# Performance work log

Measured on AMD Instinct MI355X. Metric: run time of the kernel, lower is better.

The kernel has to match this reference:

```python
import jax, jax.numpy as jnp
import numpy as np

N_CLUSTERS = 100
ALPHA = 1.0
NDF = 256
IN_DIM = 1024 * 8 * 8  # i3d_nch * os * os
BN, SN = 32, 64


def setup_inputs() -> dict:
    key = jax.random.key(0)
    k1, k2, k3, k4 = jax.random.split(key, 4)
    z_roi = jax.random.normal(k1, (BN, SN, IN_DIM), dtype=jnp.float32)
    mask = jnp.ones((BN, SN), dtype=bool)
    w_emb = jax.random.normal(k2, (IN_DIM, NDF), dtype=jnp.float32) * 0.02
    b_emb = jnp.zeros((NDF,), dtype=jnp.float32)
    centroids = jax.random.normal(k3, (N_CLUSTERS, NDF), dtype=jnp.float32)
    return {"z_roi": z_roi, "mask": mask, "w_emb": w_emb,
            "b_emb": b_emb, "centroids": centroids}


def _student_t(z, centroids):
    # z: [bn, sn, d]; centroids: [K, d]
    # pairwise L2 distance (NOT squared, matching torch.linalg.vector_norm)
    d2 = ((z * z).sum(-1, keepdims=True)
          + (centroids * centroids).sum(-1)
          - 2.0 * jnp.einsum("bsd,kd->bsk", z, centroids))  # [bn, sn, K]
    dist = jnp.sqrt(jnp.clip(d2, 0.0))
    s_tmp = (1.0 + dist / ALPHA) ** (-(ALPHA + 1.0) / 2.0)
    return s_tmp / s_tmp.sum(-1, keepdims=True)


def reference(z_roi, mask, w_emb, b_emb, centroids):
    # visual embedding: Linear(i3d_nch*os*os -> ndf)
    z = jnp.einsum("bsi,io->bso", z_roi, w_emb) + b_emb  # [bn, sn, ndf]
    m = mask[..., None]
    s = jnp.where(m, _student_t(z, centroids), 0.0)       # [bn, sn, K]
    z_all = jnp.where(m, z, 0.0)                           # detached copy in torch
    c = jnp.argmax(s, axis=2)                              # [bn, sn]
    return z_all, s, c
```

## Files before the change

kernel.cpp:

```cpp
#include <hip/hip_runtime.h>
#include <math.h>

#define MROWS 2048
#define NCOLS 256
#define KDIM  65536
#define NCLU  100

#define BM 128
#define BN 128
#define BK 32
#define SPLITK 16
#define KCHUNK (KDIM / SPLITK)
#define SA 132
#define SB 128

#define BMT 128
#define BNT 128
#define BKT 32
#define LDT 40

typedef _Float16 half8  __attribute__((ext_vector_type(8)));
typedef _Float16 half4v __attribute__((ext_vector_type(4)));
typedef float    f32x4  __attribute__((ext_vector_type(4)));

__global__ __launch_bounds__(256, 4)
void prep_b_kernel(const float* __restrict__ B,
                   _Float16* __restrict__ Bth, _Float16* __restrict__ Btl)
{
    __shared__ float T[64][65];
    const int t  = threadIdx.x;
    const int k0 = blockIdx.x * 64;
    const int n0 = blockIdx.y * 64;

    {
        const int kl = t >> 4;
        const int n4 = (t & 15) * 4;
        #pragma unroll
        for (int i = 0; i < 4; ++i) {
            const float4 v = *(const float4*)(B + (size_t)(k0 + kl + 16 * i) * NCOLS + n0 + n4);
            T[kl + 16 * i][n4 + 0] = v.x;
            T[kl + 16 * i][n4 + 1] = v.y;
            T[kl + 16 * i][n4 + 2] = v.z;
            T[kl + 16 * i][n4 + 3] = v.w;
        }
    }
    __syncthreads();
    {
        const int nl = t >> 2;
        const int kc = (t & 3) * 16;
        half8 h0, h1, l0, l1;
        #pragma unroll
        for (int j = 0; j < 8; ++j) {
            float v = T[kc + j][nl];
            _Float16 h = (_Float16)v;
            h0[j] = h; l0[j] = (_Float16)(v - (float)h);
            v = T[kc + 8 + j][nl];
            h = (_Float16)v;
            h1[j] = h; l1[j] = (_Float16)(v - (float)h);
        }
        const size_t off = (size_t)(n0 + nl) * KDIM + k0 + kc;
        *(half8*)(Bth + off)     = h0;
        *(half8*)(Bth + off + 8) = h1;
        *(half8*)(Btl + off)     = l0;
        *(half8*)(Btl + off + 8) = l1;
    }
}

__global__ __launch_bounds__(256, 1)
void gemm_mfma_kernel(const float* __restrict__ A,
                      const _Float16* __restrict__ Bth,
                      const _Float16* __restrict__ Btl,
                      float* __restrict__ C)
{
    __shared__ _Float16 As [BMT][LDT];
    __shared__ _Float16 Bhs[BNT][LDT];
    __shared__ _Float16 Bls[BNT][LDT];

    const int t    = threadIdx.x;
    const int lane = t & 63;
    const int wid  = t >> 6;
    const int wm   = wid >> 1;
    const int wn   = wid & 1;

    const int bm = blockIdx.x;
    const int bn = blockIdx.y;
    const int ks = blockIdx.z;

    const float*    Ab  = A   + (size_t)bm * BMT * KDIM + (size_t)ks * KCHUNK;
    const _Float16* Bhb = Bth + (size_t)bn * BNT * KDIM + (size_t)ks * KCHUNK;
    const _Float16* Blb = Btl + (size_t)bn * BNT * KDIM + (size_t)ks * KCHUNK;

    const int am  = t >> 3;
    const int ak  = (t & 7) * 4;
    const int bnr = t >> 2;
    const int bk  = (t & 3) * 8;

    f32x4 acc[4][4] = {};

    for (int kk = 0; kk < KCHUNK; kk += BKT) {
        __syncthreads();
        #pragma unroll
        for (int i = 0; i < 4; ++i) {
            const float4 v = *(const float4*)(Ab + (size_t)(am + 32 * i) * KDIM + kk + ak);
            half4v h;
            h[0] = (_Float16)v.x; h[1] = (_Float16)v.y;
            h[2] = (_Float16)v.z; h[3] = (_Float16)v.w;
            *(half4v*)&As[am + 32 * i][ak] = h;
        }
        #pragma unroll
        for (int i = 0; i < 2; ++i) {
            const int n = bnr + 64 * i;
            *(half8*)&Bhs[n][bk] = *(const half8*)(Bhb + (size_t)n * KDIM + kk + bk);
            *(half8*)&Bls[n][bk] = *(const half8*)(Blb + (size_t)n * KDIM + kk + bk);
        }
        __syncthreads();

        const int r16 = lane & 15;
        const int k8  = (lane >> 4) * 8;
        half8 av[4], bh[4], bl[4];
        #pragma unroll
        for (int mf = 0; mf < 4; ++mf)
            av[mf] = *(const half8*)&As[wm * 64 + mf * 16 + r16][k8];
        #pragma unroll
        for (int nf = 0; nf < 4; ++nf) {
            bh[nf] = *(const half8*)&Bhs[wn * 64 + nf * 16 + r16][k8];
            bl[nf] = *(const half8*)&Bls[wn * 64 + nf * 16 + r16][k8];
        }
        #pragma unroll
        for (int mf = 0; mf < 4; ++mf)
            #pragma unroll
            for (int nf = 0; nf < 4; ++nf) {
                acc[mf][nf] = __builtin_amdgcn_mfma_f32_16x16x32_f16(av[mf], bh[nf], acc[mf][nf], 0, 0, 0);
                acc[mf][nf] = __builtin_amdgcn_mfma_f32_16x16x32_f16(av[mf], bl[nf], acc[mf][nf], 0, 0, 0);
            }
    }

    const int row0 = bm * BMT + wm * 64 + (lane >> 4) * 4;
    const int col0 = bn * BNT + wn * 64 + (lane & 15);
    #pragma unroll
    for (int mf = 0; mf < 4; ++mf)
        #pragma unroll
        for (int nf = 0; nf < 4; ++nf)
            #pragma unroll
            for (int r = 0; r < 4; ++r)
                atomicAdd(&C[(size_t)(row0 + mf * 16 + r) * NCOLS + col0 + nf * 16],
                          acc[mf][nf][r]);
}

__global__ __launch_bounds__(256, 2)
void gemm_splitk_kernel(const float* __restrict__ A, const float* __restrict__ B,
                        float* __restrict__ C)
{
    __shared__ float As[BK][SA];
    __shared__ float Bs[BK][SB];

    const int t  = threadIdx.x;
    const int tx = t & 15;
    const int ty = t >> 4;

    const int bm = blockIdx.x;
    const int bn = blockIdx.y;
    const int bs = blockIdx.z;

    const float* Ab = A + (size_t)bm * BM * KDIM + (size_t)bs * KCHUNK;
    const float* Bb = B + (size_t)bs * KCHUNK * NCOLS + bn * BN;

    const int arow = t >> 3;
    const int akf4 = t & 7;
    const int bkr  = t >> 5;
    const int bnf4 = t & 31;

    float acc[8][8];
    #pragma unroll
    for (int i = 0; i < 8; ++i)
        #pragma unroll
        for (int j = 0; j < 8; ++j) acc[i][j] = 0.f;

    for (int kk = 0; kk < KCHUNK; kk += BK) {
        #pragma unroll
        for (int i = 0; i < 4; ++i) {
            const int r = arow + 32 * i;
            const float4 v = *(const float4*)(Ab + (size_t)r * KDIM + kk + akf4 * 4);
            As[akf4 * 4 + 0][r] = v.x;
            As[akf4 * 4 + 1][r] = v.y;
            As[akf4 * 4 + 2][r] = v.z;
            As[akf4 * 4 + 3][r] = v.w;
        }
        #pragma unroll
        for (int i = 0; i < 4; ++i) {
            const int r = bkr + 8 * i;
            *(float4*)&Bs[r][bnf4 * 4] =
                *(const float4*)(Bb + (size_t)(kk + r) * NCOLS + bnf4 * 4);
        }
        __syncthreads();

        #pragma unroll 8
        for (int k = 0; k < BK; ++k) {
            float a[8], b[8];
            *(float4*)&a[0] = *(const float4*)&As[k][ty * 4];
            *(float4*)&a[4] = *(const float4*)&As[k][64 + ty * 4];
            *(float4*)&b[0] = *(const float4*)&Bs[k][tx * 4];
            *(float4*)&b[4] = *(const float4*)&Bs[k][64 + tx * 4];
            #pragma unroll
            for (int i = 0; i < 8; ++i)
                #pragma unroll
                for (int j = 0; j < 8; ++j)
                    acc[i][j] = fmaf(a[i], b[j], acc[i][j]);
        }
        __syncthreads();
    }

    #pragma unroll
    for (int i = 0; i < 8; ++i) {
        const int row = bm * BM + ty * 4 + (i & 3) + 64 * (i >> 2);
        #pragma unroll
        for (int j = 0; j < 8; ++j) {
            const int col = bn * BN + tx * 4 + (j & 3) + 64 * (j >> 2);
            atomicAdd(&C[(size_t)row * NCOLS + col], acc[i][j]);
        }
    }
}

#define RPB 8

__global__ __launch_bounds__(256, 1)
void student_t_kernel(float* __restrict__ zbuf,
                      const int* __restrict__ mask,
                      const float* __restrict__ b_emb,
                      const float* __restrict__ cent,
                      float* __restrict__ s_out,
                      float* __restrict__ c_out)
{
    __shared__ float cs[50][257];
    __shared__ float zs[RPB][256];
    __shared__ float stbuf[RPB][128];
    __shared__ float c2[NCLU];
    __shared__ float z2s[RPB];
    __shared__ float redbuf[4];
    __shared__ float r_sum, r_idx;

    const int t    = threadIdx.x;
    const int wid  = t >> 6;
    const int lane = t & 63;
    const int row0 = blockIdx.x * RPB;

    const float bt = b_emb[t];

    if (t >= 100 && t < 128) {
        #pragma unroll
        for (int r = 0; r < RPB; ++r) stbuf[r][t] = 0.f;
    }

    for (int r = 0; r < RPB; ++r) {
        const int row = row0 + r;
        const float z = zbuf[(size_t)row * NCOLS + t] + bt;
        const bool m = mask[row] != 0;
        zbuf[(size_t)row * NCOLS + t] = m ? z : 0.f;
        zs[r][t] = z;
        float v = z * z;
        #pragma unroll
        for (int off = 32; off > 0; off >>= 1) v += __shfl_down(v, off, 64);
        if (lane == 0) redbuf[wid] = v;
        __syncthreads();
        if (t == 0) z2s[r] = redbuf[0] + redbuf[1] + redbuf[2] + redbuf[3];
        __syncthreads();
    }

    for (int ch = 0; ch < 2; ++ch) {
        const int kbase = ch * 50;
        for (int i = t; i < 50 * 256; i += 256) {
            const int k = i >> 8;
            const int d = i & 255;
            cs[k][d] = cent[(size_t)(kbase + k) * 256 + d];
        }
        __syncthreads();
        if (t < 50) {
            float s = 0.f;
            for (int d = 0; d < 256; ++d) s = fmaf(cs[t][d], cs[t][d], s);
            c2[kbase + t] = s;
        }
        __syncthreads();
        for (int rp = 0; rp < RPB / 2; ++rp) {
            if (t < 100) {
                const int r = rp * 2 + t / 50;
                const int k = t % 50;
                float dot = 0.f;
                for (int d = 0; d < 256; ++d)
                    dot = fmaf(zs[r][d], cs[k][d], dot);
                const float d2   = z2s[r] + c2[kbase + k] - 2.f * dot;
                const float dist = sqrtf(fmaxf(d2, 0.f));
                stbuf[r][kbase + k] = 1.f / (1.f + dist);
            }
        }
        __syncthreads();
    }

    for (int r = 0; r < RPB; ++r) {
        const int row = row0 + r;
        if (wid == 0) {
            const float v1 = stbuf[r][lane];
            const float v2 = stbuf[r][lane + 64];
            float sv = v1 + v2;
            #pragma unroll
            for (int off = 32; off > 0; off >>= 1) sv += __shfl_down(sv, off, 64);
            float mv; int mi;
            if (v2 > v1) { mv = v2; mi = lane + 64; } else { mv = v1; mi = lane; }
            #pragma unroll
            for (int off = 32; off > 0; off >>= 1) {
                const float ov = __shfl_down(mv, off, 64);
                const int   oi = __shfl_down(mi, off, 64);
                if (ov > mv || (ov == mv && oi < mi)) { mv = ov; mi = oi; }
            }
            if (lane == 0) { r_sum = sv; r_idx = (float)mi; }
        }
        __syncthreads();
        const bool m = mask[row] != 0;
        if (t < NCLU) s_out[(size_t)row * NCLU + t] = m ? stbuf[r][t] / r_sum : 0.f;
        if (t == 0)   c_out[row] = m ? r_idx : 0.f;
        __syncthreads();
    }
}

extern "C" void kernel_launch(void* const* d_in, const int* in_sizes, int n_in,
                              void* d_out, int out_size, void* d_ws, size_t ws_size,
                              hipStream_t stream)
{
    const float* z_roi = (const float*)d_in[0];
    const int*   mask  = (const int*)d_in[1];
    const float* w_emb = (const float*)d_in[2];
    const float* b_emb = (const float*)d_in[3];
    const float* cent  = (const float*)d_in[4];

    float* out   = (float*)d_out;
    float* z_all = out;
    float* s_out = out + (size_t)MROWS * NCOLS;
    float* c_out = s_out + (size_t)MROWS * NCLU;

    hipMemsetAsync(z_all, 0, (size_t)MROWS * NCOLS * sizeof(float), stream);

    const size_t bt_elems = (size_t)NCOLS * KDIM;
    const size_t ws_need  = bt_elems * 2 * sizeof(_Float16);

    if (ws_size >= ws_need) {
        _Float16* bth = (_Float16*)d_ws;
        _Float16* btl = bth + bt_elems;
        prep_b_kernel<<<dim3(KDIM / 64, NCOLS / 64), 256, 0, stream>>>(w_emb, bth, btl);
        gemm_mfma_kernel<<<dim3(MROWS / BMT, NCOLS / BNT, SPLITK), 256, 0, stream>>>(
            z_roi, bth, btl, z_all);
    } else {
        gemm_splitk_kernel<<<dim3(MROWS / BM, NCOLS / BN, SPLITK), 256, 0, stream>>>(
            z_roi, w_emb, z_all);
    }

    student_t_kernel<<<dim3(MROWS / RPB), 256, 0, stream>>>(z_all, mask, b_emb, cent,
                                                            s_out, c_out);
}
```

Before: 908.0 us.

## Double-buffer MFMA GEMM with pre-tiled swizzled B and direct global-to-LDS loads

The prep kernel now writes W as pre-tiled, XOR-swizzled 16KB tiles holding interleaved fp16 hi and lo parts. The GEMM loads each tile straight into LDS with global_load_lds and double-buffers both A and B. This lets the next K-step's loads overlap the current MFMAs and needs one barrier per step instead of two. Occupancy is raised to 2 blocks per CU, at the cost of more LDS per block.

```diff
diff --git a/kernel.cpp b/kernel.cpp
--- a/kernel.cpp
+++ b/kernel.cpp
@@ -17,64 +17,67 @@
 #define BMT 128
 #define BNT 128
 #define BKT 32
+#define NSTEP (KCHUNK / BKT)
 #define LDT 40
+#define BTILE 16384
 
 typedef _Float16 half8  __attribute__((ext_vector_type(8)));
 typedef _Float16 half4v __attribute__((ext_vector_type(4)));
 typedef float    f32x4  __attribute__((ext_vector_type(4)));
 
+#define GLD_LDS16(g, l) __builtin_amdgcn_global_load_lds(                      \
+    (__attribute__((address_space(1))) void*)(g),                              \
+    (__attribute__((address_space(3))) void*)(l), 16, 0, 0)
+
 __global__ __launch_bounds__(256, 4)
-void prep_b_kernel(const float* __restrict__ B,
-                   _Float16* __restrict__ Bth, _Float16* __restrict__ Btl)
-{
-    __shared__ float T[64][65];
-    const int t  = threadIdx.x;
-    const int k0 = blockIdx.x * 64;
-    const int n0 = blockIdx.y * 64;
-
-    {
-        const int kl = t >> 4;
-        const int n4 = (t & 15) * 4;
-        #pragma unroll
-        for (int i = 0; i < 4; ++i) {
-            const float4 v = *(const float4*)(B + (size_t)(k0 + kl + 16 * i) * NCOLS + n0 + n4);
-            T[kl + 16 * i][n4 + 0] = v.x;
-            T[kl + 16 * i][n4 + 1] = v.y;
-            T[kl + 16 * i][n4 + 2] = v.z;
-            T[kl + 16 * i][n4 + 3] = v.w;
-        }
+void prep_b_kernel(const float* __restrict__ B, unsigned char* __restrict__ Bws)
+{
+    __shared__ float Ts[BKT][132];
+    const int t    = threadIdx.x;
+    const int step = blockIdx.x;
+    const int ks   = blockIdx.y;
+    const int bnb  = blockIdx.z;
+
+    const int kbase = ks * KCHUNK + step * BKT;
+    const int nbase = bnb * 128;
+
+    #pragma unroll
+    for (int r = 0; r < 4; ++r) {
+        const int fidx = r * 256 + t;
+        const int k  = fidx >> 5;
+        const int c4 = fidx & 31;
+        const float4 v = *(const float4*)(B + (size_t)(kbase + k) * NCOLS + nbase + c4 * 4);
+        *(float4*)&Ts[k][c4 * 4] = v;
     }
     __syncthreads();
-    {
-        const int nl = t >> 2;
-        const int kc = (t & 3) * 16;
-        half8 h0, h1, l0, l1;
+
+    unsigned char* outT = Bws + (size_t)((bnb * SPLITK + ks) * NSTEP + step) * BTILE;
+    #pragma unroll
+    for (int r = 0; r < 4; ++r) {
+        const int oidx = r * 256 + t;
+        const int n  = oidx >> 3;
+        const int X  = oidx & 7;
+        const int LX = X ^ (n & 7);
+        const int mtx = LX >> 2;
+        const int kb  = (LX & 3) * 8;
+        half8 hv;
         #pragma unroll
         for (int j = 0; j < 8; ++j) {
-            float v = T[kc + j][nl];
-            _Float16 h = (_Float16)v;
-            h0[j] = h; l0[j] = (_Float16)(v - (float)h);
-            v = T[kc + 8 + j][nl];
-            h = (_Float16)v;
-            h1[j] = h; l1[j] = (_Float16)(v - (float)h);
-        }
-        const size_t off = (size_t)(n0 + nl) * KDIM + k0 + kc;
-        *(half8*)(Bth + off)     = h0;
-        *(half8*)(Bth + off + 8) = h1;
-        *(half8*)(Btl + off)     = l0;
-        *(half8*)(Btl + off + 8) = l1;
-    }
-}
-
-__global__ __launch_bounds__(256, 1)
+            const float v = Ts[kb + j][n];
+            const _Float16 h = (_Float16)v;
+            hv[j] = mtx ? (_Float16)(v - (float)h) : h;
+        }
+        *(half8*)(outT + n * 128 + X * 16) = hv;
+    }
+}
+
+__global__ __launch_bounds__(256, 2)
 void gemm_mfma_kernel(const float* __restrict__ A,
-                      const _Float16* __restrict__ Bth,
-                      const _Float16* __restrict__ Btl,
+                      const unsigned char* __restrict__ Bws,
                       float* __restrict__ C)
 {
-    __shared__ _Float16 As [BMT][LDT];
-    __shared__ _Float16 Bhs[BNT][LDT];
-    __shared__ _Float16 Bls[BNT][LDT];
+    __shared__ _Float16 As[2][BMT][LDT];
+    __shared__ __align__(16) unsigned char Bs[2][BTILE];
 
     const int t    = threadIdx.x;
     const int lane = t & 63;
@@ -82,49 +85,72 @@
     const int wm   = wid >> 1;
     const int wn   = wid & 1;
 
-    const int bm = blockIdx.x;
-    const int bn = blockIdx.y;
-    const int ks = blockIdx.z;
-
-    const float*    Ab  = A   + (size_t)bm * BMT * KDIM + (size_t)ks * KCHUNK;
-    const _Float16* Bhb = Bth + (size_t)bn * BNT * KDIM + (size_t)ks * KCHUNK;
-    const _Float16* Blb = Btl + (size_t)bn * BNT * KDIM + (size_t)ks * KCHUNK;
+    const int bm  = blockIdx.x;
+    const int bnb = blockIdx.y;
+    const int ks  = blockIdx.z;
+
+    const float* Ab = A + (size_t)bm * BMT * KDIM + (size_t)ks * KCHUNK;
+    const unsigned char* Bb = Bws + (size_t)((bnb * SPLITK + ks) * NSTEP) * BTILE;
 
     const int am  = t >> 3;
-    const int ak  = (t & 7) * 4;
-    const int bnr = t >> 2;
-    const int bk  = (t & 3) * 8;
+    const int akf = (t & 7) * 4;
+
+    const int r16  = lane & 15;
+    const int kb16 = lane >> 4;
+
+    int bhoff[4], bloff[4];
+    #pragma unroll
+    for (int nf = 0; nf < 4; ++nf) {
+        const int n    = wn * 64 + nf * 16 + r16;
+        const int mask = (n & 7) << 4;
+        bhoff[nf] = n * 128 + ((kb16 * 16) ^ mask);
+        bloff[nf] = n * 128 + ((64 + kb16 * 16) ^ mask);
+    }
 
     f32x4 acc[4][4] = {};
-
-    for (int kk = 0; kk < KCHUNK; kk += BKT) {
-        __syncthreads();
-        #pragma unroll
-        for (int i = 0; i < 4; ++i) {
-            const float4 v = *(const float4*)(Ab + (size_t)(am + 32 * i) * KDIM + kk + ak);
-            half4v h;
-            h[0] = (_Float16)v.x; h[1] = (_Float16)v.y;
-            h[2] = (_Float16)v.z; h[3] = (_Float16)v.w;
-            *(half4v*)&As[am + 32 * i][ak] = h;
-        }
-        #pragma unroll
-        for (int i = 0; i < 2; ++i) {
-            const int n = bnr + 64 * i;
-            *(half8*)&Bhs[n][bk] = *(const half8*)(Bhb + (size_t)n * KDIM + kk + bk);
-            *(half8*)&Bls[n][bk] = *(const half8*)(Blb + (size_t)n * KDIM + kk + bk);
-        }
-        __syncthreads();
-
-        const int r16 = lane & 15;
-        const int k8  = (lane >> 4) * 8;
+    float4 pA[4];
+
+    #pragma unroll
+    for (int i = 0; i < 4; ++i)
+        pA[i] = *(const float4*)(Ab + (size_t)(am + 32 * i) * KDIM + akf);
+    #pragma unroll
+    for (int r = 0; r < 4; ++r)
+        GLD_LDS16(Bb + (size_t)(r * 256 + t) * 16,
+                  &Bs[0][(r * 256 + wid * 64) * 16]);
+    #pragma unroll
+    for (int i = 0; i < 4; ++i) {
+        half4v h;
+        h[0] = (_Float16)pA[i].x; h[1] = (_Float16)pA[i].y;
+        h[2] = (_Float16)pA[i].z; h[3] = (_Float16)pA[i].w;
+        *(half4v*)&As[0][am + 32 * i][akf] = h;
+    }
+    __syncthreads();
+
+    int cb = 0;
+    for (int step = 0; step < NSTEP; ++step) {
+        const int nb = cb ^ 1;
+        const bool pf = (step + 1) < NSTEP;
+
+        if (pf) {
+            const int kk = (step + 1) * BKT;
+            #pragma unroll
+            for (int i = 0; i < 4; ++i)
+                pA[i] = *(const float4*)(Ab + (size_t)(am + 32 * i) * KDIM + kk + akf);
+            const unsigned char* Bt = Bb + (size_t)(step + 1) * BTILE;
+            #pragma unroll
+            for (int r = 0; r < 4; ++r)
+                GLD_LDS16(Bt + (size_t)(r * 256 + t) * 16,
+                          &Bs[nb][(r * 256 + wid * 64) * 16]);
+        }
+
         half8 av[4], bh[4], bl[4];
         #pragma unroll
         for (int mf = 0; mf < 4; ++mf)
-            av[mf] = *(const half8*)&As[wm * 64 + mf * 16 + r16][k8];
+            av[mf] = *(const half8*)&As[cb][wm * 64 + mf * 16 + r16][kb16 * 8];
         #pragma unroll
         for (int nf = 0; nf < 4; ++nf) {
-            bh[nf] = *(const half8*)&Bhs[wn * 64 + nf * 16 + r16][k8];
-            bl[nf] = *(const half8*)&Bls[wn * 64 + nf * 16 + r16][k8];
+            bh[nf] = *(const half8*)&Bs[cb][bhoff[nf]];
+            bl[nf] = *(const half8*)&Bs[cb][bloff[nf]];
         }
         #pragma unroll
         for (int mf = 0; mf < 4; ++mf)
@@ -133,10 +159,22 @@
                 acc[mf][nf] = __builtin_amdgcn_mfma_f32_16x16x32_f16(av[mf], bh[nf], acc[mf][nf], 0, 0, 0);
                 acc[mf][nf] = __builtin_amdgcn_mfma_f32_16x16x32_f16(av[mf], bl[nf], acc[mf][nf], 0, 0, 0);
             }
+
+        if (pf) {
+            #pragma unroll
+            for (int i = 0; i < 4; ++i) {
+                half4v h;
+                h[0] = (_Float16)pA[i].x; h[1] = (_Float16)pA[i].y;
+                h[2] = (_Float16)pA[i].z; h[3] = (_Float16)pA[i].w;
+                *(half4v*)&As[nb][am + 32 * i][akf] = h;
+            }
+        }
+        __syncthreads();
+        cb = nb;
     }
 
     const int row0 = bm * BMT + wm * 64 + (lane >> 4) * 4;
-    const int col0 = bn * BNT + wn * 64 + (lane & 15);
+    const int col0 = bnb * BNT + wn * 64 + r16;
     #pragma unroll
     for (int mf = 0; mf < 4; ++mf)
         #pragma unroll
@@ -338,15 +376,13 @@
 
     hipMemsetAsync(z_all, 0, (size_t)MROWS * NCOLS * sizeof(float), stream);
 
-    const size_t bt_elems = (size_t)NCOLS * KDIM;
-    const size_t ws_need  = bt_elems * 2 * sizeof(_Float16);
+    const size_t ws_need = (size_t)2 * SPLITK * NSTEP * BTILE;
 
     if (ws_size >= ws_need) {
-        _Float16* bth = (_Float16*)d_ws;
-        _Float16* btl = bth + bt_elems;
-        prep_b_kernel<<<dim3(KDIM / 64, NCOLS / 64), 256, 0, stream>>>(w_emb, bth, btl);
+        unsigned char* bws = (unsigned char*)d_ws;
+        prep_b_kernel<<<dim3(NSTEP, SPLITK, 2), 256, 0, stream>>>(w_emb, bws);
         gemm_mfma_kernel<<<dim3(MROWS / BMT, NCOLS / BNT, SPLITK), 256, 0, stream>>>(
-            z_roi, bth, btl, z_all);
+            z_roi, bws, z_all);
     } else {
         gemm_splitk_kernel<<<dim3(MROWS / BM, NCOLS / BN, SPLITK), 256, 0, stream>>>(
             z_roi, w_emb, z_all);
```

Result: slower. 1.019 ms (+12.2%).
